# Kernel tuning notes

Measured on AMD Instinct MI355X. Metric: run time of the kernel, lower is better.

The kernel has to match this reference:

```python
import jax, jax.numpy as jnp
import numpy as np

TAU = 0.01          # gumbel_softmax temperature
EPS = 1e-7          # tf.keras.backend.epsilon()
DEPTH = 5
N_NODES = 2 ** DEPTH - 1   # 31 internal nodes
N_LEAVES = 2 ** DEPTH      # 32 leaves


def _build_route():
    # route[l, node + dir*N_NODES] = 1 along the root-to-leaf path of leaf l
    # (same structure old_route_to_new_route produces for a perfect tree)
    route = np.zeros((N_LEAVES, 2 * N_NODES), dtype=np.float32)
    for l in range(N_LEAVES):
        node = 0
        for d in range(DEPTH):
            bit = (l >> (DEPTH - 1 - d)) & 1  # 0 = left, 1 = right
            route[l, node + bit * N_NODES] = 1.0
            node = 2 * node + 1 + bit
    return route


def setup_inputs() -> dict:
    B, F, T = 32768, 128, 100
    key = jax.random.key(0)
    k1, k2, k3, k4 = jax.random.split(key, 4)
    x = jax.random.normal(k1, (B, F), dtype=jnp.float32)
    kernel = jax.random.normal(k2, (T, F, N_NODES), dtype=jnp.float32) * 0.1
    bias = jax.random.normal(k3, (T, N_NODES), dtype=jnp.float32) * 0.1
    leaf = jax.random.normal(k4, (T, N_LEAVES), dtype=jnp.float32)
    route = jnp.asarray(_build_route())  # [L, 2N], shared tree topology
    return {"x": x, "kernel": kernel, "bias": bias, "leaf": leaf, "route": route}


def reference(x, kernel, bias, leaf, route):
    # NodeLayer: matmul(x, concat([K, -K], 1)) + concat([b, -b], 0)
    h = jnp.einsum("bf,tfn->btn", x, kernel) + bias          # [B, T, N]
    h2 = jnp.concatenate([h, -h], axis=-1)                   # [B, T, 2N]
    # activation1: log(clip(sigmoid(clip(h/tau, -32, 32)), eps, 1))
    a1 = jnp.log(jnp.clip(jax.nn.sigmoid(jnp.clip(h2 / TAU, -32.0, 32.0)), EPS, 1.0))
    # route aggregation: sum log-probs along each root->leaf path
    r = jnp.einsum("btm,lm->btl", a1, route)                 # [B, T, L]
    # activation2: exp(clip(., -32, 0)) -> leaf routing probabilities
    probs = jnp.exp(jnp.clip(r, -32.0, 0.0))
    # weight leaf values by route probabilities, sum over leaves and trees
    return jnp.einsum("btl,tl->b", probs, leaf)              # [B] raw GBM output
```

## Files before the change

### kernel.cpp

```cpp
#include <hip/hip_runtime.h>

typedef _Float16 f16x8  __attribute__((ext_vector_type(8)));
typedef float    f32x16 __attribute__((ext_vector_type(16)));
typedef float    f32x4  __attribute__((ext_vector_type(4)));

#define NTREES  100
#define WAVES   8
#define NCH     13
#define BM      128
#define NT      4
#define KS      9
#define TSTRIDE (KS * 512)
#define NSCALE  (-144.269504088896f)

__device__ __forceinline__ int node_of_row(int sr, float& sg) {
  const int h   = (sr >> 2) & 1;
  const int reg = (sr & 3) + ((sr >> 3) << 2);
  sg = 1.0f;
  if (reg == 0) { if (h) sg = -1.0f; return 0; }
  if (reg == 1) return 1 + h;
  if (reg < 4)  return 1 + 2 * h + reg;
  if (reg < 8)  return 3 + 4 * h + reg;
  return 7 + 8 * h + reg;
}

__device__ __forceinline__ float exp2_fast(float v) {
#if __has_builtin(__builtin_amdgcn_exp2f)
  return __builtin_amdgcn_exp2f(v);
#else
  return exp2f(v);
#endif
}

__device__ __forceinline__ float sigl(float zn) {
  float e = exp2_fast(zn);
  return __builtin_amdgcn_rcpf(1.0f + e);
}

__global__ void prep_b(const float* __restrict__ kern, const float* __restrict__ bias,
                       unsigned short* __restrict__ bws) {
  __shared__ float kt[128][32];
  __shared__ float bs[32];
  const int t = blockIdx.x, tid = threadIdx.x;
  const float* src = kern + (size_t)t * (128 * 31);
  for (int i = tid; i < 128 * 32; i += 512) {
    const int f = i >> 5, sr_ = i & 31;
    float sg; const int g = node_of_row(sr_, sg);
    kt[f][sr_] = src[f * 31 + g] * (NSCALE * sg);
  }
  if (tid < 32) {
    float sg; const int g = node_of_row(tid, sg);
    bs[tid] = bias[t * 31 + g] * (NSCALE * sg);
  }
  __syncthreads();
  unsigned short* dst = bws + (size_t)t * TSTRIDE;
  for (int s = tid; s < KS * 64; s += 512) {
    const int ks = s >> 6, lane = s & 63;
    const int row = lane & 31;
    const int k0 = ks * 16 + ((lane >> 5) << 3);
    f16x8 o;
    if (ks < 8) {
      #pragma unroll
      for (int j = 0; j < 8; ++j) o[j] = (_Float16)kt[k0 + j][row];
    } else {
      #pragma unroll
      for (int j = 0; j < 8; ++j) o[j] = (_Float16)0.0f;
      if (lane < 32) o[0] = (_Float16)bs[row];
    }
    *(f16x8*)(dst + s * 8) = o;
  }
}

__device__ __forceinline__ float half_eval(const f32x16& a, const f32x4& L0,
                                           const f32x4& L1, const f32x4& L2,
                                           const f32x4& L3) {
  float sl, sr;
  const float c0 = sigl(a[0]);
  sl = sigl(a[1]); sr = 1.0f - sl;
  const float a0 = c0 * sl, a1 = c0 * sr;
  sl = sigl(a[2]); sr = 1.0f - sl;
  const float b0 = a0 * sl, b1 = a0 * sr;
  sl = sigl(a[3]); sr = 1.0f - sl;
  const float b2 = a1 * sl, b3 = a1 * sr;
  float cum[8];
  sl = sigl(a[4]); sr = 1.0f - sl; cum[0] = b0 * sl; cum[1] = b0 * sr;
  sl = sigl(a[5]); sr = 1.0f - sl; cum[2] = b1 * sl; cum[3] = b1 * sr;
  sl = sigl(a[6]); sr = 1.0f - sl; cum[4] = b2 * sl; cum[5] = b2 * sr;
  sl = sigl(a[7]); sr = 1.0f - sl; cum[6] = b3 * sl; cum[7] = b3 * sr;
  float s = 0.0f;
  s = fmaf(cum[0], fmaf(sigl(a[8]),  L0[0] - L0[1], L0[1]), s);
  s = fmaf(cum[1], fmaf(sigl(a[9]),  L0[2] - L0[3], L0[3]), s);
  s = fmaf(cum[2], fmaf(sigl(a[10]), L1[0] - L1[1], L1[1]), s);
  s = fmaf(cum[3], fmaf(sigl(a[11]), L1[2] - L1[3], L1[3]), s);
  s = fmaf(cum[4], fmaf(sigl(a[12]), L2[0] - L2[1], L2[1]), s);
  s = fmaf(cum[5], fmaf(sigl(a[13]), L2[2] - L2[3], L2[3]), s);
  s = fmaf(cum[6], fmaf(sigl(a[14]), L3[0] - L3[1], L3[1]), s);
  s = fmaf(cum[7], fmaf(sigl(a[15]), L3[2] - L3[3], L3[3]), s);
  return s;
}

__global__ __launch_bounds__(512, 2) void gbm_main(
    const float* __restrict__ x,
    const unsigned short* __restrict__ bws,
    const float* __restrict__ leaf,
    float* __restrict__ out)
{
  __shared__ __align__(16) unsigned char lds[NT * KS * 64 * 16];
  float* red = (float*)lds;

  const int tid  = threadIdx.x;
  const int lane = tid & 63;
  const int w    = tid >> 6;
  const int rowbase = blockIdx.x * BM;

  #pragma unroll
  for (int T = 0; T < NT; ++T)
    for (int s = tid; s < KS * 64; s += 512) {
      const int ks = s >> 6, l = s & 63;
      f16x8 h8;
      if (ks < 8) {
        const int xrow = (l & 31) + T * 32;
        const int k0 = ks * 16 + ((l >> 5) << 3);
        const float* px = x + (size_t)(rowbase + xrow) * 128 + k0;
        float4 v0 = *(const float4*)px;
        float4 v1 = *(const float4*)(px + 4);
        h8[0] = (_Float16)v0.x; h8[1] = (_Float16)v0.y;
        h8[2] = (_Float16)v0.z; h8[3] = (_Float16)v0.w;
        h8[4] = (_Float16)v1.x; h8[5] = (_Float16)v1.y;
        h8[6] = (_Float16)v1.z; h8[7] = (_Float16)v1.w;
      } else {
        #pragma unroll
        for (int j = 0; j < 8; ++j) h8[j] = (_Float16)0.0f;
        if (l < 32) h8[0] = (_Float16)1.0f;
      }
      *(f16x8*)(lds + T * (KS * 64 * 16) + s * 16) = h8;
    }

  f16x8 br[KS];
  {
    const unsigned short* bt = bws + (size_t)w * TSTRIDE;
    #pragma unroll
    for (int i = 0; i < KS; ++i)
      br[i] = *(const f16x8*)(bt + (size_t)i * 512 + lane * 8);
  }

  __syncthreads();

  const int h = lane >> 5;
  float outAcc[NT] = {0.0f, 0.0f, 0.0f, 0.0f};

  for (int c = 0; c < NCH; ++c) {
    const int tree = c * WAVES + w;
    const bool act = tree < NTREES;

    f32x16 acc[NT] = {};
    if (act) {
      __builtin_amdgcn_s_setprio(1);
      #pragma unroll
      for (int ks = 0; ks < KS; ++ks) {
        #pragma unroll
        for (int T = 0; T < NT; ++T) {
          f16x8 bx = *(const f16x8*)(lds + T * (KS * 64 * 16) + (ks * 64 + lane) * 16);
          acc[T] = __builtin_amdgcn_mfma_f32_32x32x16_f16(br[ks], bx, acc[T], 0, 0, 0);
        }
      }
      __builtin_amdgcn_s_setprio(0);
    }

    if ((c + 1) * WAVES + w < NTREES) {
      const unsigned short* nb = bws + (size_t)((c + 1) * WAVES + w) * TSTRIDE;
      #pragma unroll
      for (int i = 0; i < KS; ++i)
        br[i] = *(const f16x8*)(nb + (size_t)i * 512 + lane * 8);
    }

    if (act) {
      const float* lp = leaf + (size_t)tree * 32 + (h << 4);
      f32x4 L0 = *(const f32x4*)lp;
      f32x4 L1 = *(const f32x4*)(lp + 4);
      f32x4 L2 = *(const f32x4*)(lp + 8);
      f32x4 L3 = *(const f32x4*)(lp + 12);

      #pragma unroll
      for (int T = 0; T < NT; ++T)
        outAcc[T] += half_eval(acc[T], L0, L1, L2, L3);
    }
  }

  __syncthreads();
  #pragma unroll
  for (int T = 0; T < NT; ++T)
    red[T * 512 + tid] = outAcc[T];
  __syncthreads();
  if (tid < BM) {
    const int tile = tid >> 5, r = tid & 31;
    float s = 0.0f;
    #pragma unroll
    for (int j = 0; j < 16; ++j)
      s += red[tile * 512 + j * 32 + r];
    out[rowbase + tid] = s;
  }
}

extern "C" void kernel_launch(void* const* d_in, const int* in_sizes, int n_in,
                              void* d_out, int out_size, void* d_ws, size_t ws_size,
                              hipStream_t stream) {
  const float* x    = (const float*)d_in[0];
  const float* kern = (const float*)d_in[1];
  const float* bias = (const float*)d_in[2];
  const float* leaf = (const float*)d_in[3];

  unsigned short* bws = (unsigned short*)d_ws;

  prep_b<<<NTREES, 512, 0, stream>>>(kern, bias, bws);
  gbm_main<<<32768 / BM, 512, 0, stream>>>(x, bws, leaf, (float*)d_out);
}
```

Baseline: 51.80 us.

## Keep x tiles in registers and interleave MFMA with sigmoid epilogue in two halves

The x fragments are now loaded from LDS into registers once, before the tree loop, instead of being re-read from LDS for every tree. The constant bias column becomes a register-built vector, and the LDS tile drops to 8 k-steps. The MFMA work is split into two pairs of row tiles so the sigmoid/leaf epilogue of the first pair can overlap the matrix ops of the second. Leaf differences are precomputed once per tree. This adds 32 f16x8 registers per lane, which raises register pressure under launch_bounds(512,2) and could cause spills.

```diff
diff --git a/kernel.cpp b/kernel.cpp
--- a/kernel.cpp
+++ b/kernel.cpp
@@ -9,8 +9,8 @@
 #define NCH     13
 #define BM      128
 #define NT      4
-#define KS      9
-#define TSTRIDE (KS * 512)
+#define KSX     8
+#define TSTRIDE (9 * 512)
 #define NSCALE  (-144.269504088896f)
 
 __device__ __forceinline__ int node_of_row(int sr, float& sg) {
@@ -54,7 +54,7 @@
   }
   __syncthreads();
   unsigned short* dst = bws + (size_t)t * TSTRIDE;
-  for (int s = tid; s < KS * 64; s += 512) {
+  for (int s = tid; s < 9 * 64; s += 512) {
     const int ks = s >> 6, lane = s & 63;
     const int row = lane & 31;
     const int k0 = ks * 16 + ((lane >> 5) << 3);
@@ -71,9 +71,8 @@
   }
 }
 
-__device__ __forceinline__ float half_eval(const f32x16& a, const f32x4& L0,
-                                           const f32x4& L1, const f32x4& L2,
-                                           const f32x4& L3) {
+__device__ __forceinline__ float half_eval(const f32x16& a, const float lb[8],
+                                           const float ld[8]) {
   float sl, sr;
   const float c0 = sigl(a[0]);
   sl = sigl(a[1]); sr = 1.0f - sl;
@@ -88,14 +87,9 @@
   sl = sigl(a[6]); sr = 1.0f - sl; cum[4] = b2 * sl; cum[5] = b2 * sr;
   sl = sigl(a[7]); sr = 1.0f - sl; cum[6] = b3 * sl; cum[7] = b3 * sr;
   float s = 0.0f;
-  s = fmaf(cum[0], fmaf(sigl(a[8]),  L0[0] - L0[1], L0[1]), s);
-  s = fmaf(cum[1], fmaf(sigl(a[9]),  L0[2] - L0[3], L0[3]), s);
-  s = fmaf(cum[2], fmaf(sigl(a[10]), L1[0] - L1[1], L1[1]), s);
-  s = fmaf(cum[3], fmaf(sigl(a[11]), L1[2] - L1[3], L1[3]), s);
-  s = fmaf(cum[4], fmaf(sigl(a[12]), L2[0] - L2[1], L2[1]), s);
-  s = fmaf(cum[5], fmaf(sigl(a[13]), L2[2] - L2[3], L2[3]), s);
-  s = fmaf(cum[6], fmaf(sigl(a[14]), L3[0] - L3[1], L3[1]), s);
-  s = fmaf(cum[7], fmaf(sigl(a[15]), L3[2] - L3[3], L3[3]), s);
+  #pragma unroll
+  for (int i = 0; i < 8; ++i)
+    s = fmaf(cum[i], fmaf(sigl(a[8 + i]), ld[i], lb[i]), s);
   return s;
 }
 
@@ -105,7 +99,7 @@
     const float* __restrict__ leaf,
     float* __restrict__ out)
 {
-  __shared__ __align__(16) unsigned char lds[NT * KS * 64 * 16];
+  __shared__ __align__(16) unsigned char lds[NT * KSX * 64 * 16];
   float* red = (float*)lds;
 
   const int tid  = threadIdx.x;
@@ -115,36 +109,41 @@
 
   #pragma unroll
   for (int T = 0; T < NT; ++T)
-    for (int s = tid; s < KS * 64; s += 512) {
+    for (int s = tid; s < KSX * 64; s += 512) {
       const int ks = s >> 6, l = s & 63;
+      const int xrow = (l & 31) + T * 32;
+      const int k0 = ks * 16 + ((l >> 5) << 3);
+      const float* px = x + (size_t)(rowbase + xrow) * 128 + k0;
+      float4 v0 = *(const float4*)px;
+      float4 v1 = *(const float4*)(px + 4);
       f16x8 h8;
-      if (ks < 8) {
-        const int xrow = (l & 31) + T * 32;
-        const int k0 = ks * 16 + ((l >> 5) << 3);
-        const float* px = x + (size_t)(rowbase + xrow) * 128 + k0;
-        float4 v0 = *(const float4*)px;
-        float4 v1 = *(const float4*)(px + 4);
-        h8[0] = (_Float16)v0.x; h8[1] = (_Float16)v0.y;
-        h8[2] = (_Float16)v0.z; h8[3] = (_Float16)v0.w;
-        h8[4] = (_Float16)v1.x; h8[5] = (_Float16)v1.y;
-        h8[6] = (_Float16)v1.z; h8[7] = (_Float16)v1.w;
-      } else {
-        #pragma unroll
-        for (int j = 0; j < 8; ++j) h8[j] = (_Float16)0.0f;
-        if (l < 32) h8[0] = (_Float16)1.0f;
-      }
-      *(f16x8*)(lds + T * (KS * 64 * 16) + s * 16) = h8;
+      h8[0] = (_Float16)v0.x; h8[1] = (_Float16)v0.y;
+      h8[2] = (_Float16)v0.z; h8[3] = (_Float16)v0.w;
+      h8[4] = (_Float16)v1.x; h8[5] = (_Float16)v1.y;
+      h8[6] = (_Float16)v1.z; h8[7] = (_Float16)v1.w;
+      *(f16x8*)(lds + T * (KSX * 64 * 16) + s * 16) = h8;
     }
-
-  f16x8 br[KS];
+  __syncthreads();
+
+  f16x8 bx[NT][KSX];
+  #pragma unroll
+  for (int T = 0; T < NT; ++T)
+    #pragma unroll
+    for (int ks = 0; ks < KSX; ++ks)
+      bx[T][ks] = *(const f16x8*)(lds + T * (KSX * 64 * 16) + (ks * 64 + lane) * 16);
+
+  f16x8 bxb;
+  #pragma unroll
+  for (int j = 0; j < 8; ++j) bxb[j] = (_Float16)0.0f;
+  if (lane < 32) bxb[0] = (_Float16)1.0f;
+
+  f16x8 br[9];
   {
     const unsigned short* bt = bws + (size_t)w * TSTRIDE;
     #pragma unroll
-    for (int i = 0; i < KS; ++i)
+    for (int i = 0; i < 9; ++i)
       br[i] = *(const f16x8*)(bt + (size_t)i * 512 + lane * 8);
   }
-
-  __syncthreads();
 
   const int h = lane >> 5;
   float outAcc[NT] = {0.0f, 0.0f, 0.0f, 0.0f};
@@ -153,37 +152,55 @@
     const int tree = c * WAVES + w;
     const bool act = tree < NTREES;
 
-    f32x16 acc[NT] = {};
-    if (act) {
-      __builtin_amdgcn_s_setprio(1);
-      #pragma unroll
-      for (int ks = 0; ks < KS; ++ks) {
-        #pragma unroll
-        for (int T = 0; T < NT; ++T) {
-          f16x8 bx = *(const f16x8*)(lds + T * (KS * 64 * 16) + (ks * 64 + lane) * 16);
-          acc[T] = __builtin_amdgcn_mfma_f32_32x32x16_f16(br[ks], bx, acc[T], 0, 0, 0);
-        }
-      }
-      __builtin_amdgcn_s_setprio(0);
-    }
-
-    if ((c + 1) * WAVES + w < NTREES) {
-      const unsigned short* nb = bws + (size_t)((c + 1) * WAVES + w) * TSTRIDE;
-      #pragma unroll
-      for (int i = 0; i < KS; ++i)
-        br[i] = *(const f16x8*)(nb + (size_t)i * 512 + lane * 8);
-    }
-
     if (act) {
       const float* lp = leaf + (size_t)tree * 32 + (h << 4);
-      f32x4 L0 = *(const f32x4*)lp;
-      f32x4 L1 = *(const f32x4*)(lp + 4);
-      f32x4 L2 = *(const f32x4*)(lp + 8);
-      f32x4 L3 = *(const f32x4*)(lp + 12);
-
-      #pragma unroll
-      for (int T = 0; T < NT; ++T)
-        outAcc[T] += half_eval(acc[T], L0, L1, L2, L3);
+      float lb[8], ld[8];
+      #pragma unroll
+      for (int i = 0; i < 4; ++i) {
+        f32x4 L = *(const f32x4*)(lp + i * 4);
+        lb[2 * i]     = L[1]; ld[2 * i]     = L[0] - L[1];
+        lb[2 * i + 1] = L[3]; ld[2 * i + 1] = L[2] - L[3];
+      }
+
+      f32x16 a0 = {}, a1 = {};
+      __builtin_amdgcn_s_setprio(1);
+      #pragma unroll
+      for (int ks = 0; ks < KSX; ++ks) {
+        a0 = __builtin_amdgcn_mfma_f32_32x32x16_f16(br[ks], bx[0][ks], a0, 0, 0, 0);
+        a1 = __builtin_amdgcn_mfma_f32_32x32x16_f16(br[ks], bx[1][ks], a1, 0, 0, 0);
+      }
+      a0 = __builtin_amdgcn_mfma_f32_32x32x16_f16(br[8], bxb, a0, 0, 0, 0);
+      a1 = __builtin_amdgcn_mfma_f32_32x32x16_f16(br[8], bxb, a1, 0, 0, 0);
+      __builtin_amdgcn_s_setprio(0);
+
+      outAcc[0] += half_eval(a0, lb, ld);
+      outAcc[1] += half_eval(a1, lb, ld);
+
+      f32x16 a2 = {}, a3 = {};
+      __builtin_amdgcn_s_setprio(1);
+      #pragma unroll
+      for (int ks = 0; ks < KSX; ++ks) {
+        a2 = __builtin_amdgcn_mfma_f32_32x32x16_f16(br[ks], bx[2][ks], a2, 0, 0, 0);
+        a3 = __builtin_amdgcn_mfma_f32_32x32x16_f16(br[ks], bx[3][ks], a3, 0, 0, 0);
+      }
+      a2 = __builtin_amdgcn_mfma_f32_32x32x16_f16(br[8], bxb, a2, 0, 0, 0);
+      a3 = __builtin_amdgcn_mfma_f32_32x32x16_f16(br[8], bxb, a3, 0, 0, 0);
+      __builtin_amdgcn_s_setprio(0);
+
+      if ((c + 1) * WAVES + w < NTREES) {
+        const unsigned short* nb = bws + (size_t)((c + 1) * WAVES + w) * TSTRIDE;
+        #pragma unroll
+        for (int i = 0; i < 9; ++i)
+          br[i] = *(const f16x8*)(nb + (size_t)i * 512 + lane * 8);
+      }
+
+      outAcc[2] += half_eval(a2, lb, ld);
+      outAcc[3] += half_eval(a3, lb, ld);
+    } else if ((c + 1) * WAVES + w < NTREES) {
+      const unsigned short* nb = bws + (size_t)((c + 1) * WAVES + w) * TSTRIDE;
+      #pragma unroll
+      for (int i = 0; i < 9; ++i)
+        br[i] = *(const f16x8*)(nb + (size_t)i * 512 + lane * 8);
     }
   }
 
```

Result: slower. 56.38 us (+8.8%).
